# Kernel tuning notes

Measured on AMD Instinct MI355X. Metric: run time of the kernel, lower is better.

The kernel has to match this reference:

```python
import jax, jax.numpy as jnp
import numpy as np

N_CELLS = 50000
IN_DIM = 2000
H_DIM = 128
Z_DIM = 64
N_PROTO = 32
N_CLASSES = 8
B = 64  # number of samples (ragged groups)


def _xavier(key, shape):
    fan_out, fan_in = shape
    std = jnp.sqrt(2.0 / (fan_in + fan_out))
    return std * jax.random.normal(key, shape, dtype=jnp.float32)


def setup_inputs() -> dict:
    key = jax.random.key(0)
    ks = jax.random.split(key, 16)
    x = jax.random.normal(ks[0], (N_CELLS, IN_DIM), dtype=jnp.float32)
    y = jax.random.randint(ks[1], (B,), 0, N_CLASSES)
    # sorted segment ids emulating split_idx over B ragged groups; every group non-empty
    seg = jnp.sort(jax.random.randint(ks[2], (N_CELLS - B,), 0, B))
    segment_ids = jnp.sort(jnp.concatenate([jnp.arange(B, dtype=seg.dtype), seg])).astype(jnp.int32)
    return {
        "x": x,
        "y": y,
        "segment_ids": segment_ids,
        "enc_i_w": _xavier(ks[3], (H_DIM, IN_DIM)),
        "enc_i_b": jnp.zeros((H_DIM,), jnp.float32),
        "enc_h0_w": _xavier(ks[4], (H_DIM, H_DIM)),
        "enc_h0_b": jnp.zeros((H_DIM,), jnp.float32),
        "enc_z_w": _xavier(ks[5], (Z_DIM, H_DIM)),
        "enc_z_b": jnp.zeros((Z_DIM,), jnp.float32),
        "imp_i_w": _xavier(ks[6], (H_DIM, IN_DIM)),
        "imp_i_b": jnp.zeros((H_DIM,), jnp.float32),
        "imp_h0_w": _xavier(ks[7], (H_DIM, H_DIM)),
        "imp_h0_b": jnp.zeros((H_DIM,), jnp.float32),
        "imp_p_w": _xavier(ks[8], (N_PROTO * N_CLASSES, H_DIM)),
        "imp_p_b": jnp.zeros((N_PROTO * N_CLASSES,), jnp.float32),
        "prototypes": _xavier(ks[9], (N_PROTO, Z_DIM)),
    }


def _linear(x, w, b):
    # torch nn.Linear: y = x @ w.T + b
    return x @ w.T + b


def reference(x, y, segment_ids,
              enc_i_w, enc_i_b, enc_h0_w, enc_h0_b, enc_z_w, enc_z_b,
              imp_i_w, imp_i_b, imp_h0_w, imp_h0_b, imp_p_w, imp_p_b,
              prototypes):
    act = jax.nn.leaky_relu  # slope 0.01, matches nn.LeakyReLU default
    # encode
    h = act(_linear(x, enc_i_w, enc_i_b))
    h = act(_linear(h, enc_h0_w, enc_h0_b))
    z = act(_linear(h, enc_z_w, enc_z_b))  # [N, Z]
    # importance scores
    hi = act(_linear(x, imp_i_w, imp_i_b))
    hi = act(_linear(hi, imp_h0_w, imp_h0_b))
    imp = jax.nn.sigmoid(_linear(hi, imp_p_w, imp_p_b)).reshape(-1, N_PROTO, N_CLASSES)  # [N, P, C]
    # squared euclidean cell-to-prototype distances [N, P]
    c2p = jnp.sum((z[:, None, :] - prototypes[None, :, :]) ** 2, axis=-1)
    sim = 1.0 / (c2p + 0.5)  # [N, P]
    c_logits = jnp.einsum('np,npc->nc', sim, imp)  # [N, C]
    # ragged per-sample mean (segment mean over split_idx groups)
    sums = jax.ops.segment_sum(c_logits, segment_ids, num_segments=B)
    counts = jax.ops.segment_sum(jnp.ones((c_logits.shape[0],), c_logits.dtype), segment_ids, num_segments=B)
    logits = sums / counts[:, None]  # [B, C]
    # mean cross-entropy
    logp = jax.nn.log_softmax(logits, axis=-1)
    clf_loss = -jnp.mean(jnp.take_along_axis(logp, y[:, None], axis=1))
    total_loss = clf_loss  # ct is None -> ct_loss = 0
    return total_loss, logits
```

## Files before the change

### kernel.cpp

```cpp
#include <hip/hip_runtime.h>
#include <math.h>

#define N_CELLS 50000
#define KDIM    2000
#define KPAD    2048
#define BK      128
#define NCHUNK  16
#define TM      64

typedef unsigned short u16;
typedef unsigned int   u32;
typedef __attribute__((ext_vector_type(8))) short          bf16x8;
typedef __attribute__((ext_vector_type(4))) float          f32x4;
typedef __attribute__((ext_vector_type(4))) unsigned short u16x4;

__device__ __forceinline__ u16 f2bf(float f) {
  u32 u = __builtin_bit_cast(u32, f);
  return (u16)((u + 0x7FFFu + ((u >> 16) & 1u)) >> 16);
}
__device__ __forceinline__ float bf2f(u16 h) {
  u32 u = ((u32)h) << 16;
  return __builtin_bit_cast(float, u);
}

#define WS_W1     0
#define WS_W2     1048576
#define WS_W3     (WS_W2 + 65536)
#define WS_PT     (WS_W3 + 81920)
#define WS_PN     (WS_PT + 4096)
#define WS_B1     (WS_PN + 128)
#define WS_B2     (WS_B1 + 1024)
#define WS_B3     (WS_B2 + 1024)
#define WS_SEGSUM (WS_B3 + 1280)
#define WS_SEGCNT (WS_SEGSUM + 2048)

#define LDS_SEG  0
#define LDS_SA   256
#define LDS_H2   256
#define LDS_SIM  256
#define LDS_H1   34048
#define LDS_IMP  34048
#define LDS_ZB   67840
#define LDS_CL   67840
#define LDS_ZN   77056
#define LDS_TOTAL 77312

__global__ void __launch_bounds__(256) convert_kernel(
    const float* __restrict__ enc_i_w, const float* __restrict__ imp_i_w,
    const float* __restrict__ enc_h0_w, const float* __restrict__ imp_h0_w,
    const float* __restrict__ enc_z_w, const float* __restrict__ imp_p_w,
    const float* __restrict__ protos,
    const float* __restrict__ enc_i_b, const float* __restrict__ imp_i_b,
    const float* __restrict__ enc_h0_b, const float* __restrict__ imp_h0_b,
    const float* __restrict__ enc_z_b, const float* __restrict__ imp_p_b,
    char* __restrict__ ws)
{
  u16* W1 = (u16*)(ws + WS_W1);
  u16* W2 = (u16*)(ws + WS_W2);
  u16* W3 = (u16*)(ws + WS_W3);
  u16* PT = (u16*)(ws + WS_PT);
  float* PN = (float*)(ws + WS_PN);
  float* b1 = (float*)(ws + WS_B1);
  float* b2 = (float*)(ws + WS_B2);
  float* b3 = (float*)(ws + WS_B3);

  int idx = blockIdx.x * 256 + threadIdx.x;
  if (idx < 524288) {
    int r = idx >> 11, k = idx & 2047;
    float v = 0.f;
    if (k < KDIM) v = (r < 128) ? enc_i_w[r * KDIM + k] : imp_i_w[(r - 128) * KDIM + k];
    W1[((k >> 3) * 256 + r) * 8 + (k & 7)] = f2bf(v);
  } else if (idx < 557056) {
    int j = idx - 524288; int r = j >> 7, k = j & 127;
    float v = (r < 128) ? enc_h0_w[r * 128 + k] : imp_h0_w[(r - 128) * 128 + k];
    W2[j] = f2bf(v);
  } else if (idx < 598016) {
    int j = idx - 557056; int r = j >> 7, k = j & 127;
    float v = (r < 64) ? enc_z_w[r * 128 + k] : imp_p_w[(r - 64) * 128 + k];
    W3[j] = f2bf(v);
  } else if (idx < 600064) {
    int j = idx - 598016;
    PT[j] = f2bf(protos[j]);
  } else if (idx < 600096) {
    int p = idx - 600064;
    float s = 0.f;
    for (int d = 0; d < 64; ++d) { float pb = bf2f(f2bf(protos[p * 64 + d])); s += pb * pb; }
    PN[p] = s + 0.5f;
  } else if (idx < 600352) {
    int j = idx - 600096;
    b1[j] = (j < 128) ? enc_i_b[j] : imp_i_b[j - 128];
  } else if (idx < 600608) {
    int j = idx - 600352;
    b2[j] = (j < 128) ? enc_h0_b[j] : imp_h0_b[j - 128];
  } else if (idx < 600928) {
    int j = idx - 600608;
    b3[j] = (j < 64) ? enc_z_b[j] : imp_p_b[j - 64];
  }
}

#define MFMA(a, b, c) __builtin_amdgcn_mfma_f32_16x16x32_bf16((a), (b), (c), 0, 0, 0)
#define LD8(p) (*(const bf16x8*)(const void*)(p))

#define A_GLOAD(dst_, t_) {                                                  \
  const int kb_ = (t_) * BK;                                                 \
  _Pragma("unroll")                                                          \
  for (int j_ = 0; j_ < 4; ++j_) {                                           \
    const int col_ = kb_ + (ac + 8 * j_) * 4;                                \
    dst_[j_] = (arow_ok && col_ < KDIM)                                      \
               ? __builtin_nontemporal_load((const f32x4*)(xr + col_))       \
               : f4z;                                                        \
  } }

#define A_STORE(src_, buf_) {                                                \
  u16* da_ = saB + (buf_) * (TM * BK) + ar * BK;                             \
  _Pragma("unroll")                                                          \
  for (int j_ = 0; j_ < 4; ++j_) {                                           \
    u16x4 pk_;                                                               \
    pk_[0] = f2bf(src_[j_][0]); pk_[1] = f2bf(src_[j_][1]);                  \
    pk_[2] = f2bf(src_[j_][2]); pk_[3] = f2bf(src_[j_][3]);                  \
    const int cu_ = ((ac + 8 * j_) * 4) ^ swW;                               \
    *(u16x4*)(void*)(da_ + cu_) = pk_;                                       \
  } }

#define BLOAD(t_) {                                                          \
  const int tc_ = (t_);                                                      \
  _Pragma("unroll")                                                          \
  for (int q_ = 0; q_ < 8; ++q_)                                             \
    bR[q_] = LD8(bbase + (size_t)(tc_ * 16 + (q_ >> 1) * 4) * 2048 +         \
                 (q_ & 1) * 128);                                            \
  }

#define G1_MFMA(saP_) {                                                      \
  __builtin_amdgcn_s_setprio(1);                                             \
  _Pragma("unroll")                                                          \
  for (int kk_ = 0; kk_ < 4; ++kk_) {                                        \
    const int co_ = (kk_ * 32 + l4 * 8) ^ swR;                               \
    bf16x8 af0 = LD8((saP_) + (l15)      * BK + co_);                        \
    bf16x8 af1 = LD8((saP_) + (16 + l15) * BK + co_);                        \
    bf16x8 af2 = LD8((saP_) + (32 + l15) * BK + co_);                        \
    bf16x8 af3 = LD8((saP_) + (48 + l15) * BK + co_);                        \
    acc1[0][0] = MFMA(af0, bR[kk_*2+0], acc1[0][0]);                         \
    acc1[0][1] = MFMA(af0, bR[kk_*2+1], acc1[0][1]);                         \
    acc1[1][0] = MFMA(af1, bR[kk_*2+0], acc1[1][0]);                         \
    acc1[1][1] = MFMA(af1, bR[kk_*2+1], acc1[1][1]);                         \
    acc1[2][0] = MFMA(af2, bR[kk_*2+0], acc1[2][0]);                         \
    acc1[2][1] = MFMA(af2, bR[kk_*2+1], acc1[2][1]);                         \
    acc1[3][0] = MFMA(af3, bR[kk_*2+0], acc1[3][0]);                         \
    acc1[3][1] = MFMA(af3, bR[kk_*2+1], acc1[3][1]);                         \
  }                                                                          \
  __builtin_amdgcn_s_setprio(0);                                             \
  }

__global__ void __launch_bounds__(512, 4) fused_main(
    const float* __restrict__ x, const int* __restrict__ seg,
    const char* __restrict__ ws,
    float* __restrict__ seg_sums, float* __restrict__ seg_counts)
{
  extern __shared__ char smem[];
  const int tid  = threadIdx.x;
  const int wave = tid >> 6;
  const int lane = tid & 63;
  const int l15  = lane & 15;
  const int l4   = lane >> 4;
  const int row0 = blockIdx.x * TM;
  int valid = N_CELLS - row0; if (valid > TM) valid = TM;
  const int wn0 = wave * 32;
  const int ar = tid >> 3;
  const int ac = tid & 7;
  const int swW = (ar & 7) << 3;
  const int swR = (l15 & 7) << 3;
  const f32x4 f4z = (f32x4){0.f, 0.f, 0.f, 0.f};

  if (tid < TM) {
    int r = row0 + tid;
    ((int*)(smem + LDS_SEG))[tid] = (r < N_CELLS) ? seg[r] : 0;
  }

  u16* const saB = (u16*)(smem + LDS_SA);
  const bool arow_ok = (row0 + ar) < N_CELLS;
  const float* xr = x + (size_t)(arow_ok ? (row0 + ar) : 0) * KDIM;
  const u16* const w1t = (const u16*)(ws + WS_W1);
  const u16* const bbase = w1t + (size_t)(l4 * 256 + wn0 + l15) * 8;

  f32x4 aR[4];
  bf16x8 bR[8];
  f32x4 acc1[4][2];
#pragma unroll
  for (int m = 0; m < 4; ++m)
#pragma unroll
    for (int n = 0; n < 2; ++n) acc1[m][n] = (f32x4){0.f, 0.f, 0.f, 0.f};

  A_GLOAD(aR, 0);
  A_STORE(aR, 0);
  __syncthreads();

  int cur = 0;
  for (int t = 0; t < NCHUNK; ++t) {
    BLOAD(t);
    if (t + 1 < NCHUNK) A_GLOAD(aR, t + 1);
    G1_MFMA(saB + cur * (TM * BK));
    if (t + 1 < NCHUNK) A_STORE(aR, cur ^ 1);
    __syncthreads();
    cur ^= 1;
  }

  u16* h1 = (u16*)(smem + LDS_H1);
  {
    const float* b1 = (const float*)(ws + WS_B1);
#pragma unroll
    for (int n = 0; n < 2; ++n) {
      const int col = wn0 + n * 16 + l15;
      const float bias = b1[col];
#pragma unroll
      for (int m = 0; m < 4; ++m)
#pragma unroll
        for (int j = 0; j < 4; ++j) {
          const int row = m * 16 + l4 * 4 + j;
          float v = acc1[m][n][j] + bias;
          v = (v > 0.f) ? v : 0.01f * v;
          h1[row * 264 + col] = f2bf(v);
        }
    }
  }
  __syncthreads();

  u16* h2 = (u16*)(smem + LDS_H2);
  {
    const u16* W2 = (const u16*)(ws + WS_W2);
    const int branch = wave >> 2;
    f32x4 acc2[4][2];
#pragma unroll
    for (int m = 0; m < 4; ++m)
#pragma unroll
      for (int n = 0; n < 2; ++n) acc2[m][n] = (f32x4){0.f, 0.f, 0.f, 0.f};
#pragma unroll
    for (int kk = 0; kk < 4; ++kk) {
      const int ko = kk * 32 + l4 * 8;
      bf16x8 af[4], bfr[2];
#pragma unroll
      for (int m = 0; m < 4; ++m) af[m] = LD8(h1 + (m * 16 + l15) * 264 + branch * 128 + ko);
#pragma unroll
      for (int n = 0; n < 2; ++n) bfr[n] = LD8(W2 + (wn0 + n * 16 + l15) * 128 + ko);
#pragma unroll
      for (int m = 0; m < 4; ++m)
#pragma unroll
        for (int n = 0; n < 2; ++n) acc2[m][n] = MFMA(af[m], bfr[n], acc2[m][n]);
    }
    const float* b2 = (const float*)(ws + WS_B2);
#pragma unroll
    for (int n = 0; n < 2; ++n) {
      const int col = wn0 + n * 16 + l15;
      const float bias = b2[col];
#pragma unroll
      for (int m = 0; m < 4; ++m)
#pragma unroll
        for (int j = 0; j < 4; ++j) {
          const int row = m * 16 + l4 * 4 + j;
          float v = acc2[m][n][j] + bias;
          v = (v > 0.f) ? v : 0.01f * v;
          h2[row * 264 + col] = f2bf(v);
        }
    }
  }
  __syncthreads();

  {
    const u16* W3 = (const u16*)(ws + WS_W3);
    const float* b3 = (const float*)(ws + WS_B3);
    f32x4 acc3[4][2];
#pragma unroll
    for (int m = 0; m < 4; ++m)
#pragma unroll
      for (int n = 0; n < 2; ++n) acc3[m][n] = (f32x4){0.f, 0.f, 0.f, 0.f};
#pragma unroll
    for (int kk = 0; kk < 4; ++kk) {
      const int ko = kk * 32 + l4 * 8;
      bf16x8 af[4], bfr[2];
#pragma unroll
      for (int m = 0; m < 4; ++m) af[m] = LD8(h2 + (m * 16 + l15) * 264 + 128 + ko);
#pragma unroll
      for (int n = 0; n < 2; ++n) bfr[n] = LD8(W3 + (64 + wn0 + n * 16 + l15) * 128 + ko);
#pragma unroll
      for (int m = 0; m < 4; ++m)
#pragma unroll
        for (int n = 0; n < 2; ++n) acc3[m][n] = MFMA(af[m], bfr[n], acc3[m][n]);
    }
    u16* impL = (u16*)(smem + LDS_IMP);
#pragma unroll
    for (int n = 0; n < 2; ++n) {
      const int col = wn0 + n * 16 + l15;
      const float bias = b3[64 + col];
#pragma unroll
      for (int m = 0; m < 4; ++m)
#pragma unroll
        for (int j = 0; j < 4; ++j) {
          const int row = m * 16 + l4 * 4 + j;
          float v = acc3[m][n][j] + bias;
          impL[row * 264 + col] = f2bf(1.f / (1.f + expf(-v)));
        }
    }
    if (wave < 4) {
      f32x4 accz[4];
#pragma unroll
      for (int n = 0; n < 4; ++n) accz[n] = (f32x4){0.f, 0.f, 0.f, 0.f};
#pragma unroll
      for (int kk = 0; kk < 4; ++kk) {
        const int ko = kk * 32 + l4 * 8;
        bf16x8 a = LD8(h2 + (wave * 16 + l15) * 264 + ko);
#pragma unroll
        for (int n = 0; n < 4; ++n) {
          bf16x8 b = LD8(W3 + (n * 16 + l15) * 128 + ko);
          accz[n] = MFMA(a, b, accz[n]);
        }
      }
      u16* zb = (u16*)(smem + LDS_ZB);
      float zn[4] = {0.f, 0.f, 0.f, 0.f};
#pragma unroll
      for (int n = 0; n < 4; ++n) {
        const int col = n * 16 + l15;
        const float bias = b3[col];
#pragma unroll
        for (int j = 0; j < 4; ++j) {
          const int row = wave * 16 + l4 * 4 + j;
          float v = accz[n][j] + bias;
          v = (v > 0.f) ? v : 0.01f * v;
          zb[row * 72 + col] = f2bf(v);
          zn[j] += v * v;
        }
      }
#pragma unroll
      for (int j = 0; j < 4; ++j) {
        float v = zn[j];
        v += __shfl_xor(v, 1); v += __shfl_xor(v, 2);
        v += __shfl_xor(v, 4); v += __shfl_xor(v, 8);
        zn[j] = v;
      }
      if (l15 == 0) {
        float* znL = (float*)(smem + LDS_ZN);
#pragma unroll
        for (int j = 0; j < 4; ++j) znL[wave * 16 + l4 * 4 + j] = zn[j];
      }
    }
  }
  __syncthreads();

  if (wave < 4) {
    const u16* zb = (const u16*)(smem + LDS_ZB);
    const u16* PT = (const u16*)(ws + WS_PT);
    const float* PN = (const float*)(ws + WS_PN);
    f32x4 accs[2];
#pragma unroll
    for (int n = 0; n < 2; ++n) accs[n] = (f32x4){0.f, 0.f, 0.f, 0.f};
#pragma unroll
    for (int kk = 0; kk < 2; ++kk) {
      const int ko = kk * 32 + l4 * 8;
      bf16x8 a = LD8(zb + (wave * 16 + l15) * 72 + ko);
#pragma unroll
      for (int n = 0; n < 2; ++n) {
        bf16x8 b = LD8(PT + (n * 16 + l15) * 64 + ko);
        accs[n] = MFMA(a, b, accs[n]);
      }
    }
    const float* znL = (const float*)(smem + LDS_ZN);
    float* simL = (float*)(smem + LDS_SIM);
#pragma unroll
    for (int n = 0; n < 2; ++n) {
      const int p = n * 16 + l15;
      const float pn = PN[p];
#pragma unroll
      for (int j = 0; j < 4; ++j) {
        const int row = wave * 16 + l4 * 4 + j;
        simL[row * 33 + p] = 1.f / (znL[row] - 2.f * accs[n][j] + pn);
      }
    }
  }
  __syncthreads();

  {
    const int r = tid >> 3, c = tid & 7;
    float* cl = (float*)(smem + LDS_CL);
    if (r < valid) {
      const float* simL = (const float*)(smem + LDS_SIM);
      const u16*  impL = (const u16*)(smem + LDS_IMP);
      float s = 0.f;
#pragma unroll
      for (int p = 0; p < 32; ++p) s += simL[r * 33 + p] * bf2f(impL[r * 264 + p * 8 + c]);
      cl[r * 8 + c] = s;
    }
    __syncthreads();
    if (r < valid) {
      const int* segL = (const int*)(smem + LDS_SEG);
      const int sg = segL[r];
      if (r == 0 || segL[r - 1] != sg) {
        float s = 0.f;
        int rr = r;
        do { s += cl[rr * 8 + c]; ++rr; } while (rr < valid && segL[rr] == sg);
        atomicAdd(&seg_sums[sg * 8 + c], s);
        if (c == 0) atomicAdd(&seg_counts[sg], (float)(rr - r));
      }
    }
  }
}

__global__ void __launch_bounds__(64) finalize_kernel(const char* __restrict__ ws,
                                                      const int* __restrict__ y,
                                                      float* __restrict__ out)
{
  const int b = threadIdx.x;
  const float* sums = (const float*)(ws + WS_SEGSUM);
  const float* cnts = (const float*)(ws + WS_SEGCNT);
  const float inv = 1.f / cnts[b];
  float lg[8];
  float m = -1e30f;
#pragma unroll
  for (int c = 0; c < 8; ++c) { lg[c] = sums[b * 8 + c] * inv; m = fmaxf(m, lg[c]); }
  float se = 0.f;
#pragma unroll
  for (int c = 0; c < 8; ++c) se += expf(lg[c] - m);
  const float lse = m + logf(se);
#pragma unroll
  for (int c = 0; c < 8; ++c) out[1 + b * 8 + c] = lg[c];
  const int yb = y[b];
  float part = -(lg[yb] - lse);
  for (int o = 1; o < 64; o <<= 1) part += __shfl_xor(part, o);
  if (b == 0) out[0] = part * (1.f / 64.f);
}

extern "C" void kernel_launch(void* const* d_in, const int* in_sizes, int n_in,
                              void* d_out, int out_size, void* d_ws, size_t ws_size,
                              hipStream_t stream)
{
  const float* x        = (const float*)d_in[0];
  const int*   y        = (const int*)d_in[1];
  const int*   seg      = (const int*)d_in[2];
  const float* enc_i_w  = (const float*)d_in[3];
  const float* enc_i_b  = (const float*)d_in[4];
  const float* enc_h0_w = (const float*)d_in[5];
  const float* enc_h0_b = (const float*)d_in[6];
  const float* enc_z_w  = (const float*)d_in[7];
  const float* enc_z_b  = (const float*)d_in[8];
  const float* imp_i_w  = (const float*)d_in[9];
  const float* imp_i_b  = (const float*)d_in[10];
  const float* imp_h0_w = (const float*)d_in[11];
  const float* imp_h0_b = (const float*)d_in[12];
  const float* imp_p_w  = (const float*)d_in[13];
  const float* imp_p_b  = (const float*)d_in[14];
  const float* protos   = (const float*)d_in[15];
  char* ws = (char*)d_ws;

  hipMemsetAsync(ws + WS_SEGSUM, 0, 2048 + 256, stream);

  convert_kernel<<<2348, 256, 0, stream>>>(
      enc_i_w, imp_i_w, enc_h0_w, imp_h0_w, enc_z_w, imp_p_w, protos,
      enc_i_b, imp_i_b, enc_h0_b, imp_h0_b, enc_z_b, imp_p_b, ws);

  const int nblocks = (N_CELLS + TM - 1) / TM;
  fused_main<<<nblocks, 512, LDS_TOTAL, stream>>>(
      x, seg, ws, (float*)(ws + WS_SEGSUM), (float*)(ws + WS_SEGCNT));

  finalize_kernel<<<1, 64, 0, stream>>>(ws, y, (float*)d_out);
}
```

Before: 171.2 us.

## Split fused kernel into standalone GEMM1 kernel and downstream rest kernel

The fused kernel is split in two. The first computes the large x·W1 GEMM with bias and leaky ReLU, using a small static LDS footprint and a higher occupancy hint, and writes bf16 h1 to a global workspace. The second reads h1 back into LDS and runs the remaining layers and the segment reduction. This lets the bandwidth-bound first GEMM run with more resident waves, at the cost of an extra global round trip for h1 (about 25 MB of bf16) and one more kernel launch.

```diff
diff --git a/kernel.cpp b/kernel.cpp
--- a/kernel.cpp
+++ b/kernel.cpp
@@ -7,10 +7,13 @@
 #define BK      128
 #define NCHUNK  16
 #define TM      64
+#define NTILES  782
+#define NROWPAD (NTILES * TM)
 
 typedef unsigned short u16;
 typedef unsigned int   u32;
 typedef __attribute__((ext_vector_type(8))) short          bf16x8;
+typedef __attribute__((ext_vector_type(8))) unsigned short u16x8;
 typedef __attribute__((ext_vector_type(4))) float          f32x4;
 typedef __attribute__((ext_vector_type(4))) unsigned short u16x4;
 
@@ -33,9 +36,9 @@
 #define WS_B3     (WS_B2 + 1024)
 #define WS_SEGSUM (WS_B3 + 1280)
 #define WS_SEGCNT (WS_SEGSUM + 2048)
+#define WS_H1G    (WS_SEGCNT + 256)
 
 #define LDS_SEG  0
-#define LDS_SA   256
 #define LDS_H2   256
 #define LDS_SIM  256
 #define LDS_H1   34048
@@ -151,8 +154,70 @@
   __builtin_amdgcn_s_setprio(0);                                             \
   }
 
-__global__ void __launch_bounds__(512, 4) fused_main(
-    const float* __restrict__ x, const int* __restrict__ seg,
+__global__ void __launch_bounds__(512, 6) gemm1_kernel(
+    const float* __restrict__ x, const char* __restrict__ ws,
+    u16* __restrict__ h1g)
+{
+  __shared__ u16 saB[2 * TM * BK];
+  const int tid  = threadIdx.x;
+  const int wave = tid >> 6;
+  const int lane = tid & 63;
+  const int l15  = lane & 15;
+  const int l4   = lane >> 4;
+  const int row0 = blockIdx.x * TM;
+  const int wn0  = wave * 32;
+  const int ar = tid >> 3;
+  const int ac = tid & 7;
+  const int swW = (ar & 7) << 3;
+  const int swR = (l15 & 7) << 3;
+  const f32x4 f4z = (f32x4){0.f, 0.f, 0.f, 0.f};
+
+  const bool arow_ok = (row0 + ar) < N_CELLS;
+  const float* xr = x + (size_t)(arow_ok ? (row0 + ar) : 0) * KDIM;
+  const u16* const w1t = (const u16*)(ws + WS_W1);
+  const u16* const bbase = w1t + (size_t)(l4 * 256 + wn0 + l15) * 8;
+
+  f32x4 aR[4];
+  bf16x8 bR[8];
+  f32x4 acc1[4][2];
+#pragma unroll
+  for (int m = 0; m < 4; ++m)
+#pragma unroll
+    for (int n = 0; n < 2; ++n) acc1[m][n] = (f32x4){0.f, 0.f, 0.f, 0.f};
+
+  A_GLOAD(aR, 0);
+  A_STORE(aR, 0);
+  __syncthreads();
+
+  int cur = 0;
+  for (int t = 0; t < NCHUNK; ++t) {
+    BLOAD(t);
+    if (t + 1 < NCHUNK) A_GLOAD(aR, t + 1);
+    G1_MFMA(saB + cur * (TM * BK));
+    if (t + 1 < NCHUNK) A_STORE(aR, cur ^ 1);
+    __syncthreads();
+    cur ^= 1;
+  }
+
+  const float* b1 = (const float*)(ws + WS_B1);
+#pragma unroll
+  for (int n = 0; n < 2; ++n) {
+    const int col = wn0 + n * 16 + l15;
+    const float bias = b1[col];
+#pragma unroll
+    for (int m = 0; m < 4; ++m)
+#pragma unroll
+      for (int j = 0; j < 4; ++j) {
+        const int row = m * 16 + l4 * 4 + j;
+        float v = acc1[m][n][j] + bias;
+        v = (v > 0.f) ? v : 0.01f * v;
+        h1g[(size_t)(row0 + row) * 256 + col] = f2bf(v);
+      }
+  }
+}
+
+__global__ void __launch_bounds__(512, 4) rest_kernel(
+    const u16* __restrict__ h1g, const int* __restrict__ seg,
     const char* __restrict__ ws,
     float* __restrict__ seg_sums, float* __restrict__ seg_counts)
 {
@@ -165,61 +230,20 @@
   const int row0 = blockIdx.x * TM;
   int valid = N_CELLS - row0; if (valid > TM) valid = TM;
   const int wn0 = wave * 32;
-  const int ar = tid >> 3;
-  const int ac = tid & 7;
-  const int swW = (ar & 7) << 3;
-  const int swR = (l15 & 7) << 3;
-  const f32x4 f4z = (f32x4){0.f, 0.f, 0.f, 0.f};
 
   if (tid < TM) {
     int r = row0 + tid;
     ((int*)(smem + LDS_SEG))[tid] = (r < N_CELLS) ? seg[r] : 0;
   }
 
-  u16* const saB = (u16*)(smem + LDS_SA);
-  const bool arow_ok = (row0 + ar) < N_CELLS;
-  const float* xr = x + (size_t)(arow_ok ? (row0 + ar) : 0) * KDIM;
-  const u16* const w1t = (const u16*)(ws + WS_W1);
-  const u16* const bbase = w1t + (size_t)(l4 * 256 + wn0 + l15) * 8;
-
-  f32x4 aR[4];
-  bf16x8 bR[8];
-  f32x4 acc1[4][2];
-#pragma unroll
-  for (int m = 0; m < 4; ++m)
-#pragma unroll
-    for (int n = 0; n < 2; ++n) acc1[m][n] = (f32x4){0.f, 0.f, 0.f, 0.f};
-
-  A_GLOAD(aR, 0);
-  A_STORE(aR, 0);
-  __syncthreads();
-
-  int cur = 0;
-  for (int t = 0; t < NCHUNK; ++t) {
-    BLOAD(t);
-    if (t + 1 < NCHUNK) A_GLOAD(aR, t + 1);
-    G1_MFMA(saB + cur * (TM * BK));
-    if (t + 1 < NCHUNK) A_STORE(aR, cur ^ 1);
-    __syncthreads();
-    cur ^= 1;
-  }
-
   u16* h1 = (u16*)(smem + LDS_H1);
   {
-    const float* b1 = (const float*)(ws + WS_B1);
-#pragma unroll
-    for (int n = 0; n < 2; ++n) {
-      const int col = wn0 + n * 16 + l15;
-      const float bias = b1[col];
-#pragma unroll
-      for (int m = 0; m < 4; ++m)
-#pragma unroll
-        for (int j = 0; j < 4; ++j) {
-          const int row = m * 16 + l4 * 4 + j;
-          float v = acc1[m][n][j] + bias;
-          v = (v > 0.f) ? v : 0.01f * v;
-          h1[row * 264 + col] = f2bf(v);
-        }
+    const int r = tid >> 3, c0 = (tid & 7) * 32;
+    const u16* src = h1g + (size_t)(row0 + r) * 256 + c0;
+#pragma unroll
+    for (int i = 0; i < 4; ++i) {
+      u16x8 v = *(const u16x8*)(const void*)(src + i * 8);
+      *(u16x8*)(void*)(h1 + r * 264 + c0 + i * 8) = v;
     }
   }
   __syncthreads();
@@ -454,9 +478,11 @@
       enc_i_w, imp_i_w, enc_h0_w, imp_h0_w, enc_z_w, imp_p_w, protos,
       enc_i_b, imp_i_b, enc_h0_b, imp_h0_b, enc_z_b, imp_p_b, ws);
 
-  const int nblocks = (N_CELLS + TM - 1) / TM;
-  fused_main<<<nblocks, 512, LDS_TOTAL, stream>>>(
-      x, seg, ws, (float*)(ws + WS_SEGSUM), (float*)(ws + WS_SEGCNT));
+  gemm1_kernel<<<NTILES, 512, 0, stream>>>(x, ws, (u16*)(ws + WS_H1G));
+
+  rest_kernel<<<NTILES, 512, LDS_TOTAL, stream>>>(
+      (const u16*)(ws + WS_H1G), seg, ws,
+      (float*)(ws + WS_SEGSUM), (float*)(ws + WS_SEGCNT));
 
   finalize_kernel<<<1, 64, 0, stream>>>(ws, y, (float*)d_out);
 }
```

Result: slower. 318.4 us (+86.0%).

## Prefetch A two chunks ahead and split B loads into half-chunks

Applied to the files above, without the earlier changes.

The GEMM1 main loop is unrolled by two and uses two register sets for the x tile, so global loads of x are issued two K-chunks ahead instead of one. This gives more latency hiding for the streaming fp32 input. W1 fragment loads are now done in two halves interleaved with the MFMAs, which halves the B register footprint to offset the added A registers. Register pressure under the 512-thread, 4-block launch bound could still rise and cause spills or lower occupancy.

```diff
diff --git a/kernel.cpp b/kernel.cpp
--- a/kernel.cpp
+++ b/kernel.cpp
@@ -122,31 +122,31 @@
     *(u16x4*)(void*)(da_ + cu_) = pk_;                                       \
   } }
 
-#define BLOAD(t_) {                                                          \
-  const int tc_ = (t_);                                                      \
+#define BLOADH(t_, h_) {                                                     \
   _Pragma("unroll")                                                          \
-  for (int q_ = 0; q_ < 8; ++q_)                                             \
-    bR[q_] = LD8(bbase + (size_t)(tc_ * 16 + (q_ >> 1) * 4) * 2048 +         \
-                 (q_ & 1) * 128);                                            \
-  }
-
-#define G1_MFMA(saP_) {                                                      \
+  for (int q_ = 0; q_ < 4; ++q_)                                             \
+    bR[q_] = LD8(bbase + (size_t)((t_) * 16 + ((h_) * 2 + (q_ >> 1)) * 4)    \
+                 * 2048 + (q_ & 1) * 128);                                   \
+  }
+
+#define G1_MFMA_H(saP_, h_) {                                                \
   __builtin_amdgcn_s_setprio(1);                                             \
   _Pragma("unroll")                                                          \
-  for (int kk_ = 0; kk_ < 4; ++kk_) {                                        \
+  for (int kq_ = 0; kq_ < 2; ++kq_) {                                        \
+    const int kk_ = (h_) * 2 + kq_;                                          \
     const int co_ = (kk_ * 32 + l4 * 8) ^ swR;                               \
     bf16x8 af0 = LD8((saP_) + (l15)      * BK + co_);                        \
     bf16x8 af1 = LD8((saP_) + (16 + l15) * BK + co_);                        \
     bf16x8 af2 = LD8((saP_) + (32 + l15) * BK + co_);                        \
     bf16x8 af3 = LD8((saP_) + (48 + l15) * BK + co_);                        \
-    acc1[0][0] = MFMA(af0, bR[kk_*2+0], acc1[0][0]);                         \
-    acc1[0][1] = MFMA(af0, bR[kk_*2+1], acc1[0][1]);                         \
-    acc1[1][0] = MFMA(af1, bR[kk_*2+0], acc1[1][0]);                         \
-    acc1[1][1] = MFMA(af1, bR[kk_*2+1], acc1[1][1]);                         \
-    acc1[2][0] = MFMA(af2, bR[kk_*2+0], acc1[2][0]);                         \
-    acc1[2][1] = MFMA(af2, bR[kk_*2+1], acc1[2][1]);                         \
-    acc1[3][0] = MFMA(af3, bR[kk_*2+0], acc1[3][0]);                         \
-    acc1[3][1] = MFMA(af3, bR[kk_*2+1], acc1[3][1]);                         \
+    acc1[0][0] = MFMA(af0, bR[kq_*2+0], acc1[0][0]);                         \
+    acc1[0][1] = MFMA(af0, bR[kq_*2+1], acc1[0][1]);                         \
+    acc1[1][0] = MFMA(af1, bR[kq_*2+0], acc1[1][0]);                         \
+    acc1[1][1] = MFMA(af1, bR[kq_*2+1], acc1[1][1]);                         \
+    acc1[2][0] = MFMA(af2, bR[kq_*2+0], acc1[2][0]);                         \
+    acc1[2][1] = MFMA(af2, bR[kq_*2+1], acc1[2][1]);                         \
+    acc1[3][0] = MFMA(af3, bR[kq_*2+0], acc1[3][0]);                         \
+    acc1[3][1] = MFMA(af3, bR[kq_*2+1], acc1[3][1]);                         \
   }                                                                          \
   __builtin_amdgcn_s_setprio(0);                                             \
   }
@@ -182,26 +182,34 @@
   const u16* const w1t = (const u16*)(ws + WS_W1);
   const u16* const bbase = w1t + (size_t)(l4 * 256 + wn0 + l15) * 8;
 
-  f32x4 aR[4];
-  bf16x8 bR[8];
+  f32x4 aRA[4], aRB[4];
+  bf16x8 bR[4];
   f32x4 acc1[4][2];
 #pragma unroll
   for (int m = 0; m < 4; ++m)
 #pragma unroll
     for (int n = 0; n < 2; ++n) acc1[m][n] = (f32x4){0.f, 0.f, 0.f, 0.f};
 
-  A_GLOAD(aR, 0);
-  A_STORE(aR, 0);
+  A_GLOAD(aRA, 0);
+  A_GLOAD(aRB, 1);
+  A_STORE(aRA, 0);
   __syncthreads();
 
-  int cur = 0;
-  for (int t = 0; t < NCHUNK; ++t) {
-    BLOAD(t);
-    if (t + 1 < NCHUNK) A_GLOAD(aR, t + 1);
-    G1_MFMA(saB + cur * (TM * BK));
-    if (t + 1 < NCHUNK) A_STORE(aR, cur ^ 1);
+  for (int t = 0; t < NCHUNK; t += 2) {
+    if (t + 2 < NCHUNK) A_GLOAD(aRA, t + 2);
+    BLOADH(t, 0);
+    G1_MFMA_H(saB, 0);
+    BLOADH(t, 1);
+    G1_MFMA_H(saB, 1);
+    A_STORE(aRB, 1);
     __syncthreads();
-    cur ^= 1;
+    if (t + 3 < NCHUNK) A_GLOAD(aRB, t + 3);
+    BLOADH(t + 1, 0);
+    G1_MFMA_H(saB + TM * BK, 0);
+    BLOADH(t + 1, 1);
+    G1_MFMA_H(saB + TM * BK, 1);
+    if (t + 2 < NCHUNK) A_STORE(aRA, 0);
+    __syncthreads();
   }
 
   u16* h1 = (u16*)(smem + LDS_H1);
```

Result: slower. 180.8 us (+5.6%).
